# Kernel optimization log

Hardware: AMD Instinct MI355X
Metric: run time of the kernel (lower is better)

Reference implementation:

```python
import jax, jax.numpy as jnp
import numpy as np

WS = 16          # window_size
HS = 8           # halo_size
NH = 4           # num_heads
DIM = 128
WSH = WS + 2 * HS  # 32, window with halo
B, H, W = 2, 128, 128


def _rel_pos_index():
    # static relative-position index table, (WSH^2, WSH^2), int
    r = np.arange(-HS, WS + HS)
    coords = np.stack(np.meshgrid(r, r, indexing='ij'))        # (2, WSH, WSH)
    cf = coords.reshape(2, -1)                                  # (2, WSH^2)
    rel = (cf[:, :, None] - cf[:, None, :]).transpose(1, 2, 0)  # (L, L, 2)
    rel = rel.copy()
    rel[..., 0] += WS + HS - 1
    rel[..., 1] += WS + HS - 1
    rel[..., 0] *= 2 * WS + 2 * HS - 1
    return rel.sum(-1)  # (1024, 1024)

_RPI = _rel_pos_index()


def setup_inputs() -> dict:
    key = jax.random.key(0)
    ks = jax.random.split(key, 10)
    p = lambda k, shp: (jax.random.normal(k, shp, dtype=jnp.float32) * 0.02)
    return {
        'x': jax.random.normal(ks[0], (B, H, W, DIM), dtype=jnp.float32),
        'Wq': p(ks[1], (DIM, DIM)), 'bq': jnp.zeros((DIM,), jnp.float32),
        'Wk': p(ks[2], (DIM, DIM)), 'bk': jnp.zeros((DIM,), jnp.float32),
        'Wv': p(ks[3], (DIM, DIM)), 'bv': jnp.zeros((DIM,), jnp.float32),
        'Wp': p(ks[4], (DIM, DIM)), 'bp': jnp.zeros((DIM,), jnp.float32),
        'bias_table': p(ks[5], ((2 * WS + 2 * HS - 1) ** 2, NH)),
        'shift_size': 0,
    }


def reference(x, Wq, bq, Wk, bk, Wv, bv, Wp, bp, bias_table, shift_size):
    Bx, Hx, Wx, C = x.shape
    hd = C // NH
    scale = hd ** -0.5
    if shift_size > 0:
        x = jnp.roll(x, (-shift_size, -shift_size), axis=(1, 2))
    # reflect-pad by halo and gather overlapping 32x32 windows (stride 16)
    xp = jnp.pad(x, ((0, 0), (HS, HS), (HS, HS), (0, 0)), mode='reflect')
    nWh, nWw = Hx // WS, Wx // WS
    rows = (jnp.arange(nWh) * WS)[:, None] + jnp.arange(WSH)   # (nWh, 32)
    cols = (jnp.arange(nWw) * WS)[:, None] + jnp.arange(WSH)   # (nWw, 32)
    w = xp[:, rows]                 # (B, nWh, 32, Wp, C)
    w = w[:, :, :, cols]            # (B, nWh, 32, nWw, 32, C)
    w = w.transpose(0, 1, 3, 2, 4, 5).reshape(-1, WSH, WSH, C)  # (B*nW, 32, 32, C)
    center = w[:, HS:HS + WS, HS:HS + WS].reshape(-1, WS * WS, C)   # (nWb, 256, C)
    kv = w.reshape(-1, WSH * WSH, C)                                # (nWb, 1024, C)
    q = (center @ Wq.T + bq).reshape(-1, WS * WS, NH, hd).transpose(0, 2, 1, 3)
    k = (kv @ Wk.T + bk).reshape(-1, WSH * WSH, NH, hd).transpose(0, 2, 1, 3)
    v = (kv @ Wv.T + bv).reshape(-1, WSH * WSH, NH, hd).transpose(0, 2, 1, 3)
    attn = jnp.einsum('bhqd,bhkd->bhqk', q, k) * scale   # (nWb, H, 256, 1024)
    bias = bias_table[_RPI.reshape(-1)].reshape(WSH * WSH, WSH * WSH, NH)
    bias = bias.transpose(2, 0, 1)                        # (H, 1024, 1024)
    start = HS * 2 * WS                                   # 256, as in source
    attn = attn + bias[:, start:start + WS * WS, :][None]
    attn = jax.nn.softmax(attn, axis=-1)
    out = jnp.einsum('bhqk,bhkd->bhqd', attn, v)
    out = out.transpose(0, 2, 1, 3).reshape(-1, WS * WS, C)
    out = out @ Wp.T + bp
    out = out.reshape(Bx, nWh, nWw, WS, WS, C).transpose(0, 1, 3, 2, 4, 5)
    out = out.reshape(Bx, Hx, Wx, C)
    if shift_size > 0:
        out = jnp.roll(out, (shift_size, shift_size), axis=(1, 2))
    return out
```

## Files before the change

### kernel.cpp

```cpp
#include <hip/hip_runtime.h>


typedef unsigned short ushort_t;
typedef __attribute__((ext_vector_type(8))) short bf16x8;
typedef __attribute__((ext_vector_type(4))) float floatx4;

#define NHEADS 4
#define BTBL 2209
#define PK 72
#define QSCALE 0.17677669529663687f

__device__ __forceinline__ int reflect_idx(int p) {
    p = (p < 0) ? -p : p;
    p = (p > 127) ? 254 - p : p;
    return p;
}

__device__ __forceinline__ ushort_t f2b(float x) {
    unsigned u = __float_as_uint(x);
    return (ushort_t)((u + 0x7fffu + ((u >> 16) & 1u)) >> 16);
}

__global__ __launch_bounds__(256) void pack_w(
    const float* __restrict__ Wq, const float* __restrict__ Wk,
    const float* __restrict__ Wv, const float* __restrict__ Wp,
    const float* __restrict__ bq, const float* __restrict__ bk,
    const float* __restrict__ bv, const float* __restrict__ bp,
    ushort_t* __restrict__ Wqkv, ushort_t* __restrict__ Wpb,
    float* __restrict__ bqkv, float* __restrict__ bpb)
{
    int idx = blockIdx.x * 256 + threadIdx.x;
    if (idx < 16384)       Wqkv[idx] = f2b(Wq[idx]);
    else if (idx < 32768)  Wqkv[idx] = f2b(Wk[idx - 16384]);
    else if (idx < 49152)  Wqkv[idx] = f2b(Wv[idx - 32768]);
    else if (idx < 65536)  Wpb[idx - 49152] = f2b(Wp[idx - 49152]);
    else {
        int e = idx - 65536;
        for (int k = e; k < 512; k += 256) {
            if (k < 128)      bqkv[k] = bq[k];
            else if (k < 256) bqkv[k] = bk[k - 128];
            else if (k < 384) bqkv[k] = bv[k - 256];
            else              bpb[k - 384] = bp[k - 384];
        }
    }
}

__global__ __launch_bounds__(256) void bias_frag(
    const float* __restrict__ bt, float* __restrict__ bf)
{
    int idx = blockIdx.x * 256 + threadIdx.x;
    int reg  = idx & 3;
    int lane = (idx >> 2) & 63;
    int qt   = (idx >> 8) & 15;
    int kt   = (idx >> 12) & 63;
    int h    = idx >> 18;
    int key  = kt * 16 + ((lane >> 4) << 2) + reg;
    int q    = qt * 16 + (lane & 15);
    int kr = key >> 5, kc = key & 31;
    int bidx = ((q >> 5) + 31 - kr) * 47 + (q & 31) - kc + 23;
    if (bidx < 0) bidx += BTBL;
    bf[idx] = bt[bidx * NHEADS + h];
}

template <bool IN_BF16, bool OUT_BF16>
__global__ __launch_bounds__(256) void gemm_mfma(
    const void* __restrict__ Xv, const ushort_t* __restrict__ W,
    const float* __restrict__ bias, void* __restrict__ Yv,
    const int ldy, const float scale0)
{
    __shared__ ushort_t Xs[128 * 136];

    const int t    = threadIdx.x;
    const int w    = t >> 6;
    const int lane = t & 63;
    const int quad = lane >> 4;
    const int l15  = lane & 15;
    const int m0   = blockIdx.x * 128;
    const int nb   = blockIdx.y;
    const float sc = (nb == 0) ? scale0 : 1.0f;

    if (IN_BF16) {
        const ushort_t* X = (const ushort_t*)Xv;
        #pragma unroll
        for (int i = 0; i < 8; ++i) {
            int s = t + i * 256;
            int row = s >> 4, c8 = s & 15;
            *(int4*)&Xs[row * 136 + c8 * 8] =
                *(const int4*)&X[(size_t)(m0 + row) * 128 + c8 * 8];
        }
    } else {
        const float* X = (const float*)Xv;
        #pragma unroll
        for (int i = 0; i < 16; ++i) {
            int s = t + i * 256;
            int row = s >> 5, c4 = s & 31;
            float4 v = *(const float4*)&X[(size_t)(m0 + row) * 128 + c4 * 4];
            uint2 pk;
            pk.x = (unsigned)f2b(v.x) | ((unsigned)f2b(v.y) << 16);
            pk.y = (unsigned)f2b(v.z) | ((unsigned)f2b(v.w) << 16);
            *(uint2*)&Xs[row * 136 + c4 * 4] = pk;
        }
    }
    __syncthreads();

    float bv[8];
    #pragma unroll
    for (int nt = 0; nt < 8; ++nt) bv[nt] = bias[nb * 128 + nt * 16 + l15];

    floatx4 acc[2][8];
    #pragma unroll
    for (int mt = 0; mt < 2; ++mt)
        #pragma unroll
        for (int nt = 0; nt < 8; ++nt)
            acc[mt][nt] = (floatx4)(bv[nt]);

    #pragma unroll
    for (int kc = 0; kc < 4; ++kc) {
        bf16x8 af[2], bf[8];
        #pragma unroll
        for (int mt = 0; mt < 2; ++mt)
            af[mt] = *(const bf16x8*)&Xs[(w * 32 + mt * 16 + l15) * 136 + kc * 32 + quad * 8];
        #pragma unroll
        for (int nt = 0; nt < 8; ++nt)
            bf[nt] = *(const bf16x8*)&W[(size_t)(nb * 128 + nt * 16 + l15) * 128 + kc * 32 + quad * 8];
        #pragma unroll
        for (int mt = 0; mt < 2; ++mt)
            #pragma unroll
            for (int nt = 0; nt < 8; ++nt)
                acc[mt][nt] = __builtin_amdgcn_mfma_f32_16x16x32_bf16(af[mt], bf[nt], acc[mt][nt], 0, 0, 0);
    }

    #pragma unroll
    for (int mt = 0; mt < 2; ++mt) {
        #pragma unroll
        for (int r = 0; r < 4; ++r) {
            int m = m0 + w * 32 + mt * 16 + quad * 4 + r;
            #pragma unroll
            for (int nt = 0; nt < 8; ++nt) {
                int n = nb * 128 + nt * 16 + l15;
                float y = acc[mt][nt][r] * sc;
                if (OUT_BF16)
                    ((ushort_t*)Yv)[(size_t)m * ldy + n] = f2b(y);
                else
                    ((float*)Yv)[(size_t)m * ldy + n] = y;
            }
        }
    }
}

__global__ __launch_bounds__(256, 2) void halo_attn(
    const ushort_t* __restrict__ QKV,
    const float*    __restrict__ biasf,
    ushort_t* __restrict__ O)
{
    __shared__ ushort_t P_lds[4 * 64 * PK];
    __shared__ ushort_t Vt_lds[4 * 32 * PK];

    const int t    = threadIdx.x;
    const int wave = t >> 6;
    const int lane = t & 63;
    const int quad = lane >> 4;
    const int l15  = lane & 15;

    const int win  = blockIdx.x;
    const int head = blockIdx.y;
    const int b    = win >> 6;
    const int wh   = (win >> 3) & 7;
    const int ww   = win & 7;

    bf16x8 qf[4];
    int qpix[4];
    #pragma unroll
    for (int qt = 0; qt < 4; ++qt) {
        int q_abs = wave * 64 + qt * 16 + l15;
        int gy = wh * 16 + (q_abs >> 4), gx = ww * 16 + (q_abs & 15);
        int pix = (b * 128 + gy) * 128 + gx;
        qpix[qt] = pix;
        qf[qt] = *(const bf16x8*)(QKV + (size_t)pix * 384 + head * 32 + quad * 8);
    }

    floatx4 Oa[2][4];
    #pragma unroll
    for (int dt = 0; dt < 2; ++dt)
        #pragma unroll
        for (int qt = 0; qt < 4; ++qt)
            Oa[dt][qt] = (floatx4)0.f;
    float l[4] = {0.f, 0.f, 0.f, 0.f};

    ushort_t* Pw  = P_lds  + wave * 64 * PK;
    ushort_t* Vtw = Vt_lds + wave * 32 * PK;

    for (int c = 0; c < 16; ++c) {
        {
            int keyv = c * 64 + lane;
            int ky = reflect_idx(wh * 16 + (keyv >> 5) - 8);
            int kx = reflect_idx(ww * 16 + (keyv & 31) - 8);
            int pixv = (b * 128 + ky) * 128 + kx;
            const int4* vp4 = (const int4*)(QKV + (size_t)pixv * 384 + 256 + head * 32);
            int4 vw0 = vp4[0], vw1 = vp4[1], vw2 = vp4[2], vw3 = vp4[3];
            const ushort_t* vs0 = (const ushort_t*)&vw0;
            const ushort_t* vs1 = (const ushort_t*)&vw1;
            const ushort_t* vs2 = (const ushort_t*)&vw2;
            const ushort_t* vs3 = (const ushort_t*)&vw3;
            #pragma unroll
            for (int d = 0; d < 8; ++d) {
                Vtw[(d +  0) * PK + lane] = vs0[d];
                Vtw[(d +  8) * PK + lane] = vs1[d];
                Vtw[(d + 16) * PK + lane] = vs2[d];
                Vtw[(d + 24) * PK + lane] = vs3[d];
            }
        }

        bf16x8 kf[4];
        #pragma unroll
        for (int kt = 0; kt < 4; ++kt) {
            int key = c * 64 + kt * 16 + l15;
            int ky = reflect_idx(wh * 16 + (key >> 5) - 8);
            int kx = reflect_idx(ww * 16 + (key & 31) - 8);
            int pixk = (b * 128 + ky) * 128 + kx;
            kf[kt] = *(const bf16x8*)(QKV + (size_t)pixk * 384 + 128 + head * 32 + quad * 8);
        }

        floatx4 S[4][4];
        #pragma unroll
        for (int kt = 0; kt < 4; ++kt) {
            int kt_abs = c * 4 + kt;
            #pragma unroll
            for (int qt = 0; qt < 4; ++qt) {
                size_t off = ((((size_t)head * 64 + kt_abs) * 16 + (wave * 4 + qt)) * 64 + lane) * 4;
                S[kt][qt] = *(const floatx4*)(biasf + off);
            }
        }
        #pragma unroll
        for (int kt = 0; kt < 4; ++kt)
            #pragma unroll
            for (int qt = 0; qt < 4; ++qt)
                S[kt][qt] = __builtin_amdgcn_mfma_f32_16x16x32_bf16(kf[kt], qf[qt], S[kt][qt], 0, 0, 0);

        #pragma unroll
        for (int qt = 0; qt < 4; ++qt) {
            float ls = 0.f;
            #pragma unroll
            for (int kt = 0; kt < 4; ++kt) {
                #pragma unroll
                for (int r = 0; r < 4; ++r) {
                    float p = __expf(S[kt][qt][r]);
                    S[kt][qt][r] = p;
                    ls += p;
                }
            }
            l[qt] += ls;
            #pragma unroll
            for (int kt = 0; kt < 4; ++kt) {
                uint2 pk;
                pk.x = __builtin_amdgcn_perm(__float_as_uint(S[kt][qt][1]),
                                             __float_as_uint(S[kt][qt][0]), 0x07060302u);
                pk.y = __builtin_amdgcn_perm(__float_as_uint(S[kt][qt][3]),
                                             __float_as_uint(S[kt][qt][2]), 0x07060302u);
                *(uint2*)&Pw[(qt * 16 + l15) * PK + kt * 16 + quad * 4] = pk;
            }
        }

        #pragma unroll
        for (int ks = 0; ks < 2; ++ks) {
            bf16x8 vf[2];
            #pragma unroll
            for (int dt = 0; dt < 2; ++dt)
                vf[dt] = *(const bf16x8*)&Vtw[(dt * 16 + l15) * PK + ks * 32 + quad * 8];
            #pragma unroll
            for (int qt = 0; qt < 4; ++qt) {
                bf16x8 pf = *(const bf16x8*)&Pw[(qt * 16 + l15) * PK + ks * 32 + quad * 8];
                #pragma unroll
                for (int dt = 0; dt < 2; ++dt)
                    Oa[dt][qt] = __builtin_amdgcn_mfma_f32_16x16x32_bf16(vf[dt], pf, Oa[dt][qt], 0, 0, 0);
            }
        }
    }

    #pragma unroll
    for (int qt = 0; qt < 4; ++qt) {
        float lq = l[qt];
        lq += __shfl_xor(lq, 16);
        lq += __shfl_xor(lq, 32);
        float inv = 1.0f / lq;
        #pragma unroll
        for (int dt = 0; dt < 2; ++dt) {
            uint2 pk;
            pk.x = (unsigned)f2b(Oa[dt][qt][0] * inv) | ((unsigned)f2b(Oa[dt][qt][1] * inv) << 16);
            pk.y = (unsigned)f2b(Oa[dt][qt][2] * inv) | ((unsigned)f2b(Oa[dt][qt][3] * inv) << 16);
            *(uint2*)(O + (size_t)qpix[qt] * 128 + head * 32 + dt * 16 + quad * 4) = pk;
        }
    }
}

extern "C" void kernel_launch(void* const* d_in, const int* in_sizes, int n_in,
                              void* d_out, int out_size, void* d_ws, size_t ws_size,
                              hipStream_t stream)
{
    const float* x          = (const float*)d_in[0];
    const float* Wq         = (const float*)d_in[1];
    const float* bq         = (const float*)d_in[2];
    const float* Wk         = (const float*)d_in[3];
    const float* bk         = (const float*)d_in[4];
    const float* Wv         = (const float*)d_in[5];
    const float* bv         = (const float*)d_in[6];
    const float* Wp         = (const float*)d_in[7];
    const float* bp         = (const float*)d_in[8];
    const float* bias_table = (const float*)d_in[9];
    float* out = (float*)d_out;

    const int M = 2 * 128 * 128;
    char* ws = (char*)d_ws;
    ushort_t* Wqkv = (ushort_t*)(ws);
    ushort_t* Wpb  = (ushort_t*)(ws + 98304);
    float*    bqkv = (float*)   (ws + 131072);
    float*    bpb  = (float*)   (ws + 132608);
    ushort_t* QKV  = (ushort_t*)(ws + 133120);
    ushort_t* Ob   = (ushort_t*)(ws + 25298944);
    float*    bf   = (float*)   (ws + 33687552);

    pack_w<<<dim3(257), dim3(256), 0, stream>>>(Wq, Wk, Wv, Wp, bq, bk, bv, bp,
                                                Wqkv, Wpb, bqkv, bpb);
    bias_frag<<<dim3(16384), dim3(256), 0, stream>>>(bias_table, bf);
    gemm_mfma<false, true><<<dim3(256, 3), dim3(256), 0, stream>>>(
        x, Wqkv, bqkv, QKV, 384, QSCALE);
    halo_attn<<<dim3(128, NHEADS), dim3(256), 0, stream>>>(QKV, bf, Ob);
    gemm_mfma<true, false><<<dim3(256, 1), dim3(256), 0, stream>>>(
        Ob, Wpb, bpb, out, 128, 1.0f);
}
```

Before: 173.7 us.

## Prefetch K/V/bias into registers, store bias as bf16, use exp2 softmax

The attention loop now loads the next chunk's K, V and bias fragments into registers right after the QK MFMAs, so global loads overlap the softmax and PV work. The bias fragments are stored as bf16 pre-multiplied by log2(e), which halves bias traffic and shrinks the bias_frag launch. The Q scale also folds in log2(e) so the kernel can call exp2 directly. Other changes are MFMA priority hints via s_setprio and a smaller LDS pitch (PK 72 to 66). Costs are higher register pressure and bf16 rounding of the bias, and the new pitch may cause misaligned or conflicting vector LDS reads.

Result: slower. 243.1 us (+40.0%).

```diff
diff --git a/kernel.cpp b/kernel.cpp
--- a/kernel.cpp
+++ b/kernel.cpp
@@ -7,8 +7,9 @@
 
 #define NHEADS 4
 #define BTBL 2209
-#define PK 72
-#define QSCALE 0.17677669529663687f
+#define PK 66
+#define LOG2E 1.4426950408889634f
+#define QSCALE (0.17677669529663687f * LOG2E)
 
 __device__ __forceinline__ int reflect_idx(int p) {
     p = (p < 0) ? -p : p;
@@ -46,20 +47,31 @@
 }
 
 __global__ __launch_bounds__(256) void bias_frag(
-    const float* __restrict__ bt, float* __restrict__ bf)
-{
-    int idx = blockIdx.x * 256 + threadIdx.x;
-    int reg  = idx & 3;
-    int lane = (idx >> 2) & 63;
-    int qt   = (idx >> 8) & 15;
-    int kt   = (idx >> 12) & 63;
-    int h    = idx >> 18;
-    int key  = kt * 16 + ((lane >> 4) << 2) + reg;
-    int q    = qt * 16 + (lane & 15);
-    int kr = key >> 5, kc = key & 31;
-    int bidx = ((q >> 5) + 31 - kr) * 47 + (q & 31) - kc + 23;
-    if (bidx < 0) bidx += BTBL;
-    bf[idx] = bt[bidx * NHEADS + h];
+    const float* __restrict__ bt, ushort_t* __restrict__ bf)
+{
+    int idx  = blockIdx.x * 256 + threadIdx.x;
+    int lane = idx & 63;
+    int qtw  = (idx >> 6) & 15;
+    int kt   = (idx >> 10) & 63;
+    int h    = idx >> 16;
+    int q     = qtw * 16 + (lane & 15);
+    int kbase = kt * 16 + ((lane >> 4) << 2);
+    unsigned pk0, pk1;
+    {
+        unsigned v[4];
+        #pragma unroll
+        for (int r = 0; r < 4; ++r) {
+            int key = kbase + r;
+            int kr = key >> 5, kc = key & 31;
+            int bidx = ((q >> 5) + 31 - kr) * 47 + (q & 31) - kc + 23;
+            if (bidx < 0) bidx += BTBL;
+            v[r] = f2b(bt[bidx * NHEADS + h] * LOG2E);
+        }
+        pk0 = v[0] | (v[1] << 16);
+        pk1 = v[2] | (v[3] << 16);
+    }
+    uint2 out; out.x = pk0; out.y = pk1;
+    *(uint2*)&bf[(size_t)idx * 4] = out;
 }
 
 template <bool IN_BF16, bool OUT_BF16>
@@ -150,7 +162,7 @@
 
 __global__ __launch_bounds__(256, 2) void halo_attn(
     const ushort_t* __restrict__ QKV,
-    const float*    __restrict__ biasf,
+    const ushort_t* __restrict__ biasf,
     ushort_t* __restrict__ O)
 {
     __shared__ ushort_t P_lds[4 * 64 * PK];
@@ -190,52 +202,80 @@
     ushort_t* Pw  = P_lds  + wave * 64 * PK;
     ushort_t* Vtw = Vt_lds + wave * 32 * PK;
 
+    const int kx_v = reflect_idx(ww * 16 + (lane & 31) - 8);
+    const int vsel = (lane >> 5) & 1;
+    const int kxA  = reflect_idx(ww * 16 + l15 - 8);
+    const int kxB  = reflect_idx(ww * 16 + l15 + 8);
+    const ushort_t* kbasep = QKV + 128 + head * 32 + quad * 8;
+    const ushort_t* bbase  = biasf +
+        ((((size_t)head * 64) * 16 + wave * 4) * 64 + lane) * 4;
+
+    int4    vreg[4];
+    bf16x8  kreg[4];
+    uint2   breg[16];
+
+    auto loadV = [&](int c) {
+        int ky = reflect_idx(wh * 16 + 2 * c + vsel - 8);
+        int pixv = (b * 128 + ky) * 128 + kx_v;
+        const int4* vp4 = (const int4*)(QKV + (size_t)pixv * 384 + 256 + head * 32);
+        vreg[0] = vp4[0]; vreg[1] = vp4[1]; vreg[2] = vp4[2]; vreg[3] = vp4[3];
+    };
+    auto loadK = [&](int c) {
+        int ky0 = reflect_idx(wh * 16 + 2 * c - 8);
+        int ky1 = reflect_idx(wh * 16 + 2 * c - 7);
+        kreg[0] = *(const bf16x8*)(kbasep + (size_t)((b * 128 + ky0) * 128 + kxA) * 384);
+        kreg[1] = *(const bf16x8*)(kbasep + (size_t)((b * 128 + ky0) * 128 + kxB) * 384);
+        kreg[2] = *(const bf16x8*)(kbasep + (size_t)((b * 128 + ky1) * 128 + kxA) * 384);
+        kreg[3] = *(const bf16x8*)(kbasep + (size_t)((b * 128 + ky1) * 128 + kxB) * 384);
+    };
+    auto loadB = [&](int c) {
+        #pragma unroll
+        for (int kt = 0; kt < 4; ++kt)
+            #pragma unroll
+            for (int qt = 0; qt < 4; ++qt)
+                breg[kt * 4 + qt] =
+                    *(const uint2*)(bbase + (size_t)(c * 4 + kt) * 4096 + qt * 256);
+    };
+
+    loadV(0); loadK(0); loadB(0);
+
+    #pragma unroll 1
     for (int c = 0; c < 16; ++c) {
         {
-            int keyv = c * 64 + lane;
-            int ky = reflect_idx(wh * 16 + (keyv >> 5) - 8);
-            int kx = reflect_idx(ww * 16 + (keyv & 31) - 8);
-            int pixv = (b * 128 + ky) * 128 + kx;
-            const int4* vp4 = (const int4*)(QKV + (size_t)pixv * 384 + 256 + head * 32);
-            int4 vw0 = vp4[0], vw1 = vp4[1], vw2 = vp4[2], vw3 = vp4[3];
-            const ushort_t* vs0 = (const ushort_t*)&vw0;
-            const ushort_t* vs1 = (const ushort_t*)&vw1;
-            const ushort_t* vs2 = (const ushort_t*)&vw2;
-            const ushort_t* vs3 = (const ushort_t*)&vw3;
+            const ushort_t* vs = (const ushort_t*)vreg;
             #pragma unroll
             for (int d = 0; d < 8; ++d) {
-                Vtw[(d +  0) * PK + lane] = vs0[d];
-                Vtw[(d +  8) * PK + lane] = vs1[d];
-                Vtw[(d + 16) * PK + lane] = vs2[d];
-                Vtw[(d + 24) * PK + lane] = vs3[d];
-            }
-        }
-
-        bf16x8 kf[4];
+                Vtw[(d +  0) * PK + lane] = vs[d];
+                Vtw[(d +  8) * PK + lane] = vs[8 + d];
+                Vtw[(d + 16) * PK + lane] = vs[16 + d];
+                Vtw[(d + 24) * PK + lane] = vs[24 + d];
+            }
+        }
+
+        floatx4 S[4][4];
         #pragma unroll
         for (int kt = 0; kt < 4; ++kt) {
-            int key = c * 64 + kt * 16 + l15;
-            int ky = reflect_idx(wh * 16 + (key >> 5) - 8);
-            int kx = reflect_idx(ww * 16 + (key & 31) - 8);
-            int pixk = (b * 128 + ky) * 128 + kx;
-            kf[kt] = *(const bf16x8*)(QKV + (size_t)pixk * 384 + 128 + head * 32 + quad * 8);
-        }
-
-        floatx4 S[4][4];
-        #pragma unroll
-        for (int kt = 0; kt < 4; ++kt) {
-            int kt_abs = c * 4 + kt;
             #pragma unroll
             for (int qt = 0; qt < 4; ++qt) {
-                size_t off = ((((size_t)head * 64 + kt_abs) * 16 + (wave * 4 + qt)) * 64 + lane) * 4;
-                S[kt][qt] = *(const floatx4*)(biasf + off);
-            }
-        }
+                uint2 bb = breg[kt * 4 + qt];
+                floatx4 s;
+                s[0] = __uint_as_float(bb.x << 16);
+                s[1] = __uint_as_float(bb.x & 0xffff0000u);
+                s[2] = __uint_as_float(bb.y << 16);
+                s[3] = __uint_as_float(bb.y & 0xffff0000u);
+                S[kt][qt] = s;
+            }
+        }
+        __builtin_amdgcn_s_setprio(1);
         #pragma unroll
         for (int kt = 0; kt < 4; ++kt)
             #pragma unroll
             for (int qt = 0; qt < 4; ++qt)
-                S[kt][qt] = __builtin_amdgcn_mfma_f32_16x16x32_bf16(kf[kt], qf[qt], S[kt][qt], 0, 0, 0);
+                S[kt][qt] = __builtin_amdgcn_mfma_f32_16x16x32_bf16(kreg[kt], qf[qt], S[kt][qt], 0, 0, 0);
+        __builtin_amdgcn_s_setprio(0);
+
+        int cn = (c + 1) & 15;
+        loadV(cn); loadK(cn); loadB(cn);
 
         #pragma unroll
         for (int qt = 0; qt < 4; ++qt) {
@@ -244,7 +284,7 @@
             for (int kt = 0; kt < 4; ++kt) {
                 #pragma unroll
                 for (int r = 0; r < 4; ++r) {
-                    float p = __expf(S[kt][qt][r]);
+                    float p = __builtin_amdgcn_exp2f(S[kt][qt][r]);
                     S[kt][qt][r] = p;
                     ls += p;
                 }
@@ -261,6 +301,7 @@
             }
         }
 
+        __builtin_amdgcn_s_setprio(1);
         #pragma unroll
         for (int ks = 0; ks < 2; ++ks) {
             bf16x8 vf[2];
@@ -275,6 +316,7 @@
                     Oa[dt][qt] = __builtin_amdgcn_mfma_f32_16x16x32_bf16(vf[dt], pf, Oa[dt][qt], 0, 0, 0);
             }
         }
+        __builtin_amdgcn_s_setprio(0);
     }
 
     #pragma unroll
@@ -309,7 +351,6 @@
     const float* bias_table = (const float*)d_in[9];
     float* out = (float*)d_out;
 
-    const int M = 2 * 128 * 128;
     char* ws = (char*)d_ws;
     ushort_t* Wqkv = (ushort_t*)(ws);
     ushort_t* Wpb  = (ushort_t*)(ws + 98304);
@@ -317,11 +358,11 @@
     float*    bpb  = (float*)   (ws + 132608);
     ushort_t* QKV  = (ushort_t*)(ws + 133120);
     ushort_t* Ob   = (ushort_t*)(ws + 25298944);
-    float*    bf   = (float*)   (ws + 33687552);
+    ushort_t* bf   = (ushort_t*)(ws + 33687552);
 
     pack_w<<<dim3(257), dim3(256), 0, stream>>>(Wq, Wk, Wv, Wp, bq, bk, bv, bp,
                                                 Wqkv, Wpb, bqkv, bpb);
-    bias_frag<<<dim3(16384), dim3(256), 0, stream>>>(bias_table, bf);
+    bias_frag<<<dim3(4096), dim3(256), 0, stream>>>(bias_table, bf);
     gemm_mfma<false, true><<<dim3(256, 3), dim3(256), 0, stream>>>(
         x, Wqkv, bqkv, QKV, 384, QSCALE);
     halo_attn<<<dim3(128, NHEADS), dim3(256), 0, stream>>>(QKV, bf, Ob);
```

## Store attention bias fragments in bf16 and use exp2 with log2e prescaling

Applied to the files above, without the earlier changes.

The precomputed per-fragment relative-position bias is stored as packed bf16 instead of fp32, halving the bytes each attention block streams. It is premultiplied by log2e, as is the query scale, so the softmax can use the hardware exp2 instruction instead of expf. The bias builder now writes four values per thread, and the LDS row pitch for P/V tiles shrinks. This trades bias precision, and possibly LDS alignment or bank behaviour, for lower memory traffic and cheaper exponentials.

After: 249.2 us. +43.5%, slower.

```diff
diff --git a/kernel.cpp b/kernel.cpp
--- a/kernel.cpp
+++ b/kernel.cpp
@@ -7,8 +7,9 @@
 
 #define NHEADS 4
 #define BTBL 2209
-#define PK 72
-#define QSCALE 0.17677669529663687f
+#define PK 66
+#define LOG2E 1.4426950408889634f
+#define QSCALE (0.17677669529663687f * LOG2E)
 
 __device__ __forceinline__ int reflect_idx(int p) {
     p = (p < 0) ? -p : p;
@@ -46,20 +47,28 @@
 }
 
 __global__ __launch_bounds__(256) void bias_frag(
-    const float* __restrict__ bt, float* __restrict__ bf)
-{
-    int idx = blockIdx.x * 256 + threadIdx.x;
-    int reg  = idx & 3;
-    int lane = (idx >> 2) & 63;
-    int qt   = (idx >> 8) & 15;
-    int kt   = (idx >> 12) & 63;
-    int h    = idx >> 18;
-    int key  = kt * 16 + ((lane >> 4) << 2) + reg;
-    int q    = qt * 16 + (lane & 15);
-    int kr = key >> 5, kc = key & 31;
-    int bidx = ((q >> 5) + 31 - kr) * 47 + (q & 31) - kc + 23;
-    if (bidx < 0) bidx += BTBL;
-    bf[idx] = bt[bidx * NHEADS + h];
+    const float* __restrict__ bt, ushort_t* __restrict__ bf)
+{
+    int idx  = blockIdx.x * 256 + threadIdx.x;
+    int lane = idx & 63;
+    int qtw  = (idx >> 6) & 15;
+    int kt   = (idx >> 10) & 63;
+    int h    = (idx >> 16) & 3;
+    int q     = qtw * 16 + (lane & 15);
+    int kbase = kt * 16 + ((lane >> 4) << 2);
+    unsigned v[4];
+    #pragma unroll
+    for (int r = 0; r < 4; ++r) {
+        int key = kbase + r;
+        int kr = key >> 5, kc = key & 31;
+        int bidx = ((q >> 5) + 31 - kr) * 47 + (q & 31) - kc + 23;
+        if (bidx < 0) bidx += BTBL;
+        v[r] = f2b(bt[bidx * NHEADS + h] * LOG2E);
+    }
+    uint2 out;
+    out.x = v[0] | (v[1] << 16);
+    out.y = v[2] | (v[3] << 16);
+    *(uint2*)&bf[(size_t)idx * 4] = out;
 }
 
 template <bool IN_BF16, bool OUT_BF16>
@@ -150,7 +159,7 @@
 
 __global__ __launch_bounds__(256, 2) void halo_attn(
     const ushort_t* __restrict__ QKV,
-    const float*    __restrict__ biasf,
+    const ushort_t* __restrict__ biasf,
     ushort_t* __restrict__ O)
 {
     __shared__ ushort_t P_lds[4 * 64 * PK];
@@ -228,7 +237,13 @@
             #pragma unroll
             for (int qt = 0; qt < 4; ++qt) {
                 size_t off = ((((size_t)head * 64 + kt_abs) * 16 + (wave * 4 + qt)) * 64 + lane) * 4;
-                S[kt][qt] = *(const floatx4*)(biasf + off);
+                uint2 bb = *(const uint2*)(biasf + off);
+                floatx4 s;
+                s[0] = __uint_as_float(bb.x << 16);
+                s[1] = __uint_as_float(bb.x & 0xffff0000u);
+                s[2] = __uint_as_float(bb.y << 16);
+                s[3] = __uint_as_float(bb.y & 0xffff0000u);
+                S[kt][qt] = s;
             }
         }
         #pragma unroll
@@ -244,7 +259,7 @@
             for (int kt = 0; kt < 4; ++kt) {
                 #pragma unroll
                 for (int r = 0; r < 4; ++r) {
-                    float p = __expf(S[kt][qt][r]);
+                    float p = __builtin_amdgcn_exp2f(S[kt][qt][r]);
                     S[kt][qt][r] = p;
                     ls += p;
                 }
@@ -309,7 +324,6 @@
     const float* bias_table = (const float*)d_in[9];
     float* out = (float*)d_out;
 
-    const int M = 2 * 128 * 128;
     char* ws = (char*)d_ws;
     ushort_t* Wqkv = (ushort_t*)(ws);
     ushort_t* Wpb  = (ushort_t*)(ws + 98304);
@@ -317,11 +331,11 @@
     float*    bpb  = (float*)   (ws + 132608);
     ushort_t* QKV  = (ushort_t*)(ws + 133120);
     ushort_t* Ob   = (ushort_t*)(ws + 25298944);
-    float*    bf   = (float*)   (ws + 33687552);
+    ushort_t* bf   = (ushort_t*)(ws + 33687552);
 
     pack_w<<<dim3(257), dim3(256), 0, stream>>>(Wq, Wk, Wv, Wp, bq, bk, bv, bp,
                                                 Wqkv, Wpb, bqkv, bpb);
-    bias_frag<<<dim3(16384), dim3(256), 0, stream>>>(bias_table, bf);
+    bias_frag<<<dim3(1024), dim3(256), 0, stream>>>(bias_table, bf);
     gemm_mfma<false, true><<<dim3(256, 3), dim3(256), 0, stream>>>(
         x, Wqkv, bqkv, QKV, 384, QSCALE);
     halo_attn<<<dim3(128, NHEADS), dim3(256), 0, stream>>>(QKV, bf, Ob);
```
